# Kernel optimization log

Hardware: AMD Instinct MI355X
Metric: run time of the kernel (lower is better)

## Reference

```python
import jax, jax.numpy as jnp
import numpy as np
import math

ALPHA = 0.1
LAMDA = 0.5
N_NODES = 100000
N_EDGES = 1600000
NLAYER = 4


def gcn_norm(edge_index, num_nodes):
    # symmetric GCN normalization with added self loops (fill value 1.0)
    loop = jnp.arange(num_nodes, dtype=edge_index.dtype)
    row = jnp.concatenate([edge_index[0], loop])
    col = jnp.concatenate([edge_index[1], loop])
    w = jnp.ones(row.shape[0], dtype=jnp.float32)
    deg = jax.ops.segment_sum(w, col, num_segments=num_nodes)
    dis = jnp.where(deg > 0, jax.lax.rsqrt(deg), 0.0)
    return row, col, dis[row] * w * dis[col]


def gcnii_conv(x, h0, w1, w2, beta, row, col, norm_w, num_nodes):
    # support/initial residual mixing (GCNII)
    support = (1.0 - beta) * (1.0 - ALPHA) * x + beta * (x @ w1)
    initial = (1.0 - beta) * ALPHA * h0 + beta * (h0 @ w2)
    # gather-scale-scatter: out[i] = sum_e norm_w[e] * support[row[e]] at col[e]
    msgs = norm_w[:, None] * support[row]
    agg = jax.ops.segment_sum(msgs, col, num_segments=num_nodes)
    return agg + initial


def setup_inputs() -> dict:
    key = jax.random.key(0)
    ks = jax.random.split(key, 8)
    # edges without self loops: col = (row + offset) % N, offset in [1, N-1]
    row = jax.random.randint(ks[0], (N_EDGES,), 0, N_NODES)
    off = jax.random.randint(ks[1], (N_EDGES,), 1, N_NODES)
    col = (row + off) % N_NODES
    edge_index = jnp.stack([row, col]).astype(jnp.int64)
    g = 0.1
    return {
        "x": jax.random.normal(ks[2], (N_NODES, 17), jnp.float32),
        "edge_index": edge_index,
        "W_in": jax.random.normal(ks[3], (17, 64), jnp.float32) * g,
        "b_in": jnp.zeros((64,), jnp.float32),
        "W1": jax.random.normal(ks[4], (NLAYER, 64, 64), jnp.float32) * g,
        "W2": jax.random.normal(ks[5], (NLAYER, 64, 64), jnp.float32) * g,
        "W_out": jax.random.normal(ks[6], (64, 2), jnp.float32) * g,
        "b_out": jnp.zeros((2,), jnp.float32),
    }


def reference(x, edge_index, W_in, b_in, W1, W2, W_out, b_out):
    num_nodes = x.shape[0]
    row, col, norm_w = gcn_norm(edge_index, num_nodes)
    # eval mode: dropout is identity
    h = jax.nn.relu(x @ W_in + b_in)
    h0 = h
    for i in range(NLAYER):
        beta = math.log(LAMDA / (i + 1) + 1.0)
        h = jax.nn.relu(gcnii_conv(h, h0, W1[i], W2[i], beta, row, col, norm_w, num_nodes))
    logits = h @ W_out + b_out
    return jax.nn.log_softmax(logits, axis=1)
```

## Files before the change

### kernel.cpp

```cpp
#include <hip/hip_runtime.h>
#include <math.h>

#define ALPHA_C 0.1f
#define EPB 4096

typedef __attribute__((ext_vector_type(4))) float f32x4;
typedef __attribute__((ext_vector_type(8))) short bf16x8;

__device__ __forceinline__ float readlane_f(float v, int l) {
    return __int_as_float(__builtin_amdgcn_readlane(__float_as_int(v), l));
}

__device__ __forceinline__ unsigned short bf16_rtne(float f) {
    unsigned u = __float_as_uint(f);
    unsigned r = (u + 0x7FFFu + ((u >> 16) & 1u)) >> 16;
    return (unsigned short)r;
}

__global__ void k_rhist(const int* __restrict__ col, int E, int span,
                        int* __restrict__ rangecount) {
    __shared__ int l[64];
    int tid = threadIdx.x;
    if (tid < 64) l[tid] = 0;
    __syncthreads();
    int base = blockIdx.x * EPB;
#pragma unroll
    for (int it = 0; it < 16; ++it) {
        int e = base + it * 256 + tid;
        if (e < E) atomicAdd(&l[(unsigned)col[e] / (unsigned)span], 1);
    }
    __syncthreads();
    if (tid < 64 && l[tid]) atomicAdd(&rangecount[tid], l[tid]);
}

__global__ void k_rscan(const int* __restrict__ rangecount,
                        int* __restrict__ rangeoffs, int E) {
    __shared__ int s[64];
    int tid = threadIdx.x;
    int v = rangecount[tid];
    s[tid] = v;
    __syncthreads();
    for (int d = 1; d < 64; d <<= 1) {
        int t = (tid >= d) ? s[tid - d] : 0;
        __syncthreads();
        s[tid] += t;
        __syncthreads();
    }
    rangeoffs[tid] = s[tid] - v;
    if (tid == 63) rangeoffs[64] = E;
}

__global__ void k_binA(const int* __restrict__ row, const int* __restrict__ col,
                       const int* __restrict__ rangeoffs, int* __restrict__ gcur,
                       uint2* __restrict__ staged, int E, int span) {
    __shared__ int lrun[64];
    int tid = threadIdx.x;
    int base = blockIdx.x * EPB;
    if (tid < 64) lrun[tid] = 0;
    __syncthreads();
#pragma unroll
    for (int it = 0; it < 16; ++it) {
        int e = base + it * 256 + tid;
        if (e < E) atomicAdd(&lrun[(unsigned)col[e] / (unsigned)span], 1);
    }
    __syncthreads();
    if (tid < 64) {
        int cnt = lrun[tid];
        int gb = cnt ? atomicAdd(&gcur[tid], cnt) : 0;
        lrun[tid] = rangeoffs[tid] + gb;
    }
    __syncthreads();
#pragma unroll
    for (int it = 0; it < 16; ++it) {
        int e = base + it * 256 + tid;
        if (e < E) {
            int c = col[e];
            int r = (unsigned)c / (unsigned)span;
            int pos = atomicAdd(&lrun[r], 1);
            staged[pos] = make_uint2((unsigned)c, (unsigned)row[e]);
        }
    }
}

__global__ void k_binB(const uint2* __restrict__ staged, const int* __restrict__ rangeoffs,
                       int* __restrict__ offs, float* __restrict__ dinv,
                       int* __restrict__ srcarr, int N, int span) {
    __shared__ int lcnt[1600];
    __shared__ int partial[256];
    int r = blockIdx.x;
    int tid = threadIdx.x;
    int nstart = r * span;
    if (nstart >= N) return;
    int nend = nstart + span; if (nend > N) nend = N;
    int cnt = nend - nstart;
    int estart = rangeoffs[r], eend = rangeoffs[r + 1];
    for (int t = tid; t < cnt; t += 256) lcnt[t] = 0;
    __syncthreads();
    for (int e = estart + tid; e < eend; e += 256)
        atomicAdd(&lcnt[(int)staged[e].x - nstart], 1);
    __syncthreads();
    int chunk = (cnt + 255) / 256;
    int c0 = tid * chunk; if (c0 > cnt) c0 = cnt;
    int c1 = c0 + chunk;  if (c1 > cnt) c1 = cnt;
    int sum = 0;
    for (int t = c0; t < c1; ++t) sum += lcnt[t];
    partial[tid] = sum;
    __syncthreads();
    for (int d = 1; d < 256; d <<= 1) {
        int t = (tid >= d) ? partial[tid - d] : 0;
        __syncthreads();
        partial[tid] += t;
        __syncthreads();
    }
    int run = estart + partial[tid] - sum;
    for (int t = c0; t < c1; ++t) {
        int c = lcnt[t];
        lcnt[t] = run;
        offs[nstart + t] = run;
        dinv[nstart + t] = rsqrtf(1.0f + (float)c);
        run += c;
    }
    if (nend == N && tid == 0) offs[N] = eend;
    __syncthreads();
    for (int e = estart + tid; e < eend; e += 256) {
        uint2 cr = staged[e];
        int idx = atomicAdd(&lcnt[(int)cr.x - nstart], 1);
        srcarr[idx] = (int)cr.y;
    }
}

__global__ void k_in(const float* __restrict__ x, const float* __restrict__ Win,
                     const float* __restrict__ bin, const float* __restrict__ dinv,
                     float* __restrict__ h0, unsigned short* __restrict__ g, int N) {
    int lane = threadIdx.x & 63;
    int wave = (blockIdx.x * blockDim.x + threadIdx.x) >> 6;
    int nwaves = (gridDim.x * blockDim.x) >> 6;
    float wreg[17];
#pragma unroll
    for (int k = 0; k < 17; ++k) wreg[k] = Win[k * 64 + lane];
    float breg = bin[lane];
    for (int i = wave; i < N; i += nwaves) {
        float xv = (lane < 17) ? x[i * 17 + lane] : 0.0f;
        float acc = breg;
#pragma unroll
        for (int k = 0; k < 17; ++k) acc += readlane_f(xv, k) * wreg[k];
        float r = fmaxf(acc, 0.0f);
        h0[(size_t)i * 64 + lane] = r;
        g[(size_t)i * 64 + lane] = bf16_rtne(dinv[i] * r);
    }
}

template <bool WRITE_G>
__global__ void k_gmix(const unsigned int* __restrict__ gp, const float* __restrict__ h0,
                       const float* __restrict__ W1, const float* __restrict__ W2,
                       const float* __restrict__ dinv, const int* __restrict__ offs,
                       const int* __restrict__ srcarr, float beta,
                       float* __restrict__ of32, unsigned short* __restrict__ og16,
                       int N) {
    __shared__ float atile_s[4][16][68];
    int lane = threadIdx.x & 63;
    int wv = threadIdx.x >> 6;
    float (*atile)[68] = atile_s[wv];
    int p = lane & 31, s = lane >> 5;
    int wid = (blockIdx.x * blockDim.x + threadIdx.x) >> 6;
    int nw = (gridDim.x * blockDim.x) >> 6;
    float c1 = (1.0f - beta) * (1.0f - ALPHA_C);
    float c2 = (1.0f - beta) * ALPHA_C;

    bf16x8 bfrag[4][4];
#pragma unroll
    for (int c = 0; c < 4; ++c) {
#pragma unroll
        for (int ks = 0; ks < 4; ++ks) {
            int n = c * 16 + (lane & 15);
            int kb = ks * 32 + (lane >> 4) * 8;
            bf16x8 f;
#pragma unroll
            for (int j = 0; j < 8; ++j) {
                int k = kb + j;
                float w = (k < 64) ? beta * W1[k * 64 + n]
                                   : beta * W2[(k - 64) * 64 + n];
                f[j] = (short)bf16_rtne(w);
            }
            bfrag[c][ks] = f;
        }
    }

    int ntiles = (N + 15) >> 4;
    for (int t = wid; t < ntiles; t += nw) {
        for (int ii = 0; ii < 16; ++ii) {
            int i = t * 16 + ii; if (i >= N) i = N - 1;
            int e0 = offs[i], e1 = offs[i + 1];
            float a0 = 0.0f, a1 = 0.0f;
            for (int base = e0 + s * 8; base < e1; base += 16) {
                int idx[8];
                unsigned v[8];
#pragma unroll
                for (int u = 0; u < 8; ++u) {
                    int ee = base + u;
                    idx[u] = srcarr[ee < e1 ? ee : e1 - 1];
                }
#pragma unroll
                for (int u = 0; u < 8; ++u) v[u] = gp[(size_t)idx[u] * 32 + p];
#pragma unroll
                for (int u = 0; u < 8; ++u) {
                    bool ok = (base + u < e1);
                    a0 += ok ? __uint_as_float(v[u] << 16) : 0.0f;
                    a1 += ok ? __uint_as_float(v[u] & 0xFFFF0000u) : 0.0f;
                }
            }
            a0 += __shfl_xor(a0, 32, 64);
            a1 += __shfl_xor(a1, 32, 64);
            unsigned sv = gp[(size_t)i * 32 + p];
            a0 += __uint_as_float(sv << 16);
            a1 += __uint_as_float(sv & 0xFFFF0000u);
            if (s == 0) {
                float di = dinv[i];
                atile[ii][2 * p] = di * a0;
                atile[ii][2 * p + 1] = di * a1;
            }
        }
        int rl = lane & 15;
        int koff = (lane >> 4) * 8;
        int grow = t * 16 + rl; if (grow >= N) grow = N - 1;
        f32x4 acc[4];
#pragma unroll
        for (int c = 0; c < 4; ++c) acc[c] = (f32x4){0.f, 0.f, 0.f, 0.f};
#pragma unroll
        for (int ks = 0; ks < 4; ++ks) {
            const float* sp = (ks < 2)
                ? &atile[rl][ks * 32 + koff]
                : &h0[(size_t)grow * 64 + (ks - 2) * 32 + koff];
            f32x4 lo = *(const f32x4*)sp;
            f32x4 hi = *(const f32x4*)(sp + 4);
            bf16x8 af;
#pragma unroll
            for (int j = 0; j < 4; ++j) af[j] = (short)bf16_rtne(lo[j]);
#pragma unroll
            for (int j = 0; j < 4; ++j) af[4 + j] = (short)bf16_rtne(hi[j]);
#pragma unroll
            for (int c = 0; c < 4; ++c)
                acc[c] = __builtin_amdgcn_mfma_f32_16x16x32_bf16(af, bfrag[c][ks], acc[c], 0, 0, 0);
        }
#pragma unroll
        for (int c = 0; c < 4; ++c) {
            int col = c * 16 + rl;
#pragma unroll
            for (int q = 0; q < 4; ++q) {
                int row16 = (lane >> 4) * 4 + q;
                int gr = t * 16 + row16;
                if (gr < N) {
                    float a = atile[row16][col];
                    size_t o = (size_t)gr * 64 + col;
                    float v = c1 * a + c2 * h0[o] + acc[c][q];
                    float rr = fmaxf(v, 0.0f);
                    if (WRITE_G) og16[o] = bf16_rtne(dinv[gr] * rr);
                    else         of32[o] = rr;
                }
            }
        }
    }
}

__global__ void k_out(const float* __restrict__ h, const float* __restrict__ Wout,
                      const float* __restrict__ bout, float* __restrict__ out, int N) {
    int lane = threadIdx.x & 63;
    int wave = (blockIdx.x * blockDim.x + threadIdx.x) >> 6;
    int nwaves = (gridDim.x * blockDim.x) >> 6;
    float w0 = Wout[lane * 2 + 0], w1 = Wout[lane * 2 + 1];
    float b0 = bout[0], b1 = bout[1];
    for (int i = wave; i < N; i += nwaves) {
        float hv = h[(size_t)i * 64 + lane];
        float p0 = hv * w0, p1 = hv * w1;
#pragma unroll
        for (int d = 32; d > 0; d >>= 1) {
            p0 += __shfl_xor(p0, d, 64);
            p1 += __shfl_xor(p1, d, 64);
        }
        if (lane == 0) {
            float c0 = p0 + b0, c1 = p1 + b1;
            float m = fmaxf(c0, c1);
            float lse = m + logf(expf(c0 - m) + expf(c1 - m));
            out[(size_t)i * 2 + 0] = c0 - lse;
            out[(size_t)i * 2 + 1] = c1 - lse;
        }
    }
}

extern "C" void kernel_launch(void* const* d_in, const int* in_sizes, int n_in,
                              void* d_out, int out_size, void* d_ws, size_t ws_size,
                              hipStream_t stream) {
    const float* x    = (const float*)d_in[0];
    const int*   ei   = (const int*)d_in[1];
    const float* Win  = (const float*)d_in[2];
    const float* bin  = (const float*)d_in[3];
    const float* W1   = (const float*)d_in[4];
    const float* W2   = (const float*)d_in[5];
    const float* Wout = (const float*)d_in[6];
    const float* bout = (const float*)d_in[7];
    float* out = (float*)d_out;

    const int N = in_sizes[0] / 17;
    const int E = in_sizes[1] / 2;
    const int* rowp = ei;
    const int* colp = ei + E;
    const int span = (N + 63) / 64;

    char* p = (char*)d_ws;
    auto alloc = [&](size_t bytes) -> char* {
        char* r = p;
        p += (bytes + 255) & ~(size_t)255;
        return r;
    };
    int*   offs   = (int*)alloc((size_t)(N + 1) * sizeof(int));
    float* dinv   = (float*)alloc((size_t)N * sizeof(float));
    int*   rc_gc  = (int*)alloc(128 * sizeof(int));
    int*   roffs  = (int*)alloc(65 * sizeof(int));
    int*   srcarr = (int*)alloc((size_t)E * sizeof(int));
    size_t gbytes = (size_t)N * 64 * sizeof(unsigned short);
    size_t stbytes = (size_t)E * sizeof(uint2);
    char*  stg    = alloc(stbytes > gbytes ? stbytes : gbytes);
    float* h0     = (float*)alloc((size_t)N * 64 * sizeof(float));
    float* hfin   = (float*)alloc((size_t)N * 64 * sizeof(float));
    unsigned short* gA = (unsigned short*)alloc(gbytes);
    uint2*          staged = (uint2*)stg;
    unsigned short* gB     = (unsigned short*)stg;

    int* rangecount = rc_gc;
    int* gcur       = rc_gc + 64;
    hipMemsetAsync(rc_gc, 0, 128 * sizeof(int), stream);

    const int TB = 256;
    const int nbA = (E + EPB - 1) / EPB;

    k_rhist<<<nbA, TB, 0, stream>>>(colp, E, span, rangecount);
    k_rscan<<<1, 64, 0, stream>>>(rangecount, roffs, E);
    k_binA<<<nbA, TB, 0, stream>>>(rowp, colp, roffs, gcur, staged, E, span);
    k_binB<<<64, TB, 0, stream>>>(staged, roffs, offs, dinv, srcarr, N, span);

    k_in<<<2048, TB, 0, stream>>>(x, Win, bin, dinv, h0, gA, N);

    for (int l = 0; l < 4; ++l) {
        float beta = logf(0.5f / (float)(l + 1) + 1.0f);
        const unsigned short* gin = (l & 1) ? gB : gA;
        unsigned short*       gout = (l & 1) ? gA : gB;
        if (l < 3)
            k_gmix<true><<<1024, TB, 0, stream>>>((const unsigned int*)gin, h0,
                                                  W1 + (size_t)l * 4096, W2 + (size_t)l * 4096,
                                                  dinv, offs, srcarr, beta,
                                                  nullptr, gout, N);
        else
            k_gmix<false><<<1024, TB, 0, stream>>>((const unsigned int*)gin, h0,
                                                   W1 + (size_t)l * 4096, W2 + (size_t)l * 4096,
                                                   dinv, offs, srcarr, beta,
                                                   hfin, nullptr, N);
    }
    k_out<<<1024, TB, 0, stream>>>(hfin, Wout, bout, out, N);
}
```

Measured before the change: 470.1 us.

## Store h0 in bf16, fold alpha residual into W2, one tile per wave

h0 is now stored as bf16 and loaded straight into the MFMA A fragment, which halves its memory traffic and drops the separate fp32 reload in the epilogue. The (1-beta)*alpha*h0 term is folded into the diagonal of the W2 B fragment. The grid-stride loop is replaced with one 16-row tile per wave. Each half-wave now aggregates its own node instead of splitting one node's edges across two halves, and dinv is cached in LDS. This costs some precision, since h0 and the residual coefficient now go through bf16, and it launches many more blocks, each of which rebuilds the B fragments from W1 and W2.

```diff
diff --git a/kernel.cpp b/kernel.cpp
--- a/kernel.cpp
+++ b/kernel.cpp
@@ -5,6 +5,7 @@
 #define EPB 4096
 
 typedef __attribute__((ext_vector_type(4))) float f32x4;
+typedef __attribute__((ext_vector_type(2))) float f32x2;
 typedef __attribute__((ext_vector_type(8))) short bf16x8;
 
 __device__ __forceinline__ float readlane_f(float v, int l) {
@@ -131,7 +132,8 @@
 
 __global__ void k_in(const float* __restrict__ x, const float* __restrict__ Win,
                      const float* __restrict__ bin, const float* __restrict__ dinv,
-                     float* __restrict__ h0, unsigned short* __restrict__ g, int N) {
+                     unsigned short* __restrict__ h0b, unsigned short* __restrict__ g,
+                     int N) {
     int lane = threadIdx.x & 63;
     int wave = (blockIdx.x * blockDim.x + threadIdx.x) >> 6;
     int nwaves = (gridDim.x * blockDim.x) >> 6;
@@ -145,25 +147,25 @@
 #pragma unroll
         for (int k = 0; k < 17; ++k) acc += readlane_f(xv, k) * wreg[k];
         float r = fmaxf(acc, 0.0f);
-        h0[(size_t)i * 64 + lane] = r;
+        h0b[(size_t)i * 64 + lane] = bf16_rtne(r);
         g[(size_t)i * 64 + lane] = bf16_rtne(dinv[i] * r);
     }
 }
 
 template <bool WRITE_G>
-__global__ void k_gmix(const unsigned int* __restrict__ gp, const float* __restrict__ h0,
+__global__ void k_gmix(const unsigned int* __restrict__ gp,
+                       const unsigned int* __restrict__ h0b,
                        const float* __restrict__ W1, const float* __restrict__ W2,
                        const float* __restrict__ dinv, const int* __restrict__ offs,
                        const int* __restrict__ srcarr, float beta,
                        float* __restrict__ of32, unsigned short* __restrict__ og16,
-                       int N) {
+                       int N, int ntiles) {
     __shared__ float atile_s[4][16][68];
     int lane = threadIdx.x & 63;
     int wv = threadIdx.x >> 6;
     float (*atile)[68] = atile_s[wv];
     int p = lane & 31, s = lane >> 5;
-    int wid = (blockIdx.x * blockDim.x + threadIdx.x) >> 6;
-    int nw = (gridDim.x * blockDim.x) >> 6;
+    int t = (blockIdx.x * blockDim.x + threadIdx.x) >> 6;
     float c1 = (1.0f - beta) * (1.0f - ALPHA_C);
     float c2 = (1.0f - beta) * ALPHA_C;
 
@@ -178,85 +180,86 @@
 #pragma unroll
             for (int j = 0; j < 8; ++j) {
                 int k = kb + j;
-                float w = (k < 64) ? beta * W1[k * 64 + n]
-                                   : beta * W2[(k - 64) * 64 + n];
+                float w = (k < 64)
+                    ? beta * W1[k * 64 + n]
+                    : beta * W2[(k - 64) * 64 + n] + (((k - 64) == n) ? c2 : 0.0f);
                 f[j] = (short)bf16_rtne(w);
             }
             bfrag[c][ks] = f;
         }
     }
 
-    int ntiles = (N + 15) >> 4;
-    for (int t = wid; t < ntiles; t += nw) {
-        for (int ii = 0; ii < 16; ++ii) {
-            int i = t * 16 + ii; if (i >= N) i = N - 1;
-            int e0 = offs[i], e1 = offs[i + 1];
-            float a0 = 0.0f, a1 = 0.0f;
-            for (int base = e0 + s * 8; base < e1; base += 16) {
-                int idx[8];
-                unsigned v[8];
-#pragma unroll
-                for (int u = 0; u < 8; ++u) {
-                    int ee = base + u;
-                    idx[u] = srcarr[ee < e1 ? ee : e1 - 1];
-                }
-#pragma unroll
-                for (int u = 0; u < 8; ++u) v[u] = gp[(size_t)idx[u] * 32 + p];
-#pragma unroll
-                for (int u = 0; u < 8; ++u) {
-                    bool ok = (base + u < e1);
-                    a0 += ok ? __uint_as_float(v[u] << 16) : 0.0f;
-                    a1 += ok ? __uint_as_float(v[u] & 0xFFFF0000u) : 0.0f;
-                }
+    if (t >= ntiles) return;
+
+    for (int ii = 0; ii < 8; ++ii) {
+        int i = t * 16 + 2 * ii + s; if (i >= N) i = N - 1;
+        int e0 = offs[i], e1 = offs[i + 1];
+        float a0 = 0.0f, a1 = 0.0f;
+        for (int base = e0; base < e1; base += 8) {
+            int idx[8];
+            unsigned v[8];
+#pragma unroll
+            for (int u = 0; u < 8; ++u) {
+                int ee = base + u;
+                idx[u] = srcarr[ee < e1 ? ee : e1 - 1];
             }
-            a0 += __shfl_xor(a0, 32, 64);
-            a1 += __shfl_xor(a1, 32, 64);
-            unsigned sv = gp[(size_t)i * 32 + p];
-            a0 += __uint_as_float(sv << 16);
-            a1 += __uint_as_float(sv & 0xFFFF0000u);
-            if (s == 0) {
-                float di = dinv[i];
-                atile[ii][2 * p] = di * a0;
-                atile[ii][2 * p + 1] = di * a1;
+#pragma unroll
+            for (int u = 0; u < 8; ++u) v[u] = gp[(size_t)idx[u] * 32 + p];
+#pragma unroll
+            for (int u = 0; u < 8; ++u) {
+                bool ok = (base + u < e1);
+                a0 += ok ? __uint_as_float(v[u] << 16) : 0.0f;
+                a1 += ok ? __uint_as_float(v[u] & 0xFFFF0000u) : 0.0f;
             }
         }
-        int rl = lane & 15;
-        int koff = (lane >> 4) * 8;
-        int grow = t * 16 + rl; if (grow >= N) grow = N - 1;
-        f32x4 acc[4];
-#pragma unroll
-        for (int c = 0; c < 4; ++c) acc[c] = (f32x4){0.f, 0.f, 0.f, 0.f};
-#pragma unroll
-        for (int ks = 0; ks < 4; ++ks) {
-            const float* sp = (ks < 2)
-                ? &atile[rl][ks * 32 + koff]
-                : &h0[(size_t)grow * 64 + (ks - 2) * 32 + koff];
+        unsigned sv = gp[(size_t)i * 32 + p];
+        a0 += __uint_as_float(sv << 16);
+        a1 += __uint_as_float(sv & 0xFFFF0000u);
+        float di = dinv[i];
+        int r16 = 2 * ii + s;
+        f32x2 w = {di * a0, di * a1};
+        *(f32x2*)&atile[r16][2 * p] = w;
+        if (p == 0) atile[r16][66] = di;
+    }
+
+    int rl = lane & 15;
+    int koff = (lane >> 4) * 8;
+    int grow = t * 16 + rl; if (grow >= N) grow = N - 1;
+    f32x4 acc[4];
+#pragma unroll
+    for (int c = 0; c < 4; ++c) acc[c] = (f32x4){0.f, 0.f, 0.f, 0.f};
+#pragma unroll
+    for (int ks = 0; ks < 4; ++ks) {
+        bf16x8 af;
+        if (ks < 2) {
+            const float* sp = &atile[rl][ks * 32 + koff];
             f32x4 lo = *(const f32x4*)sp;
             f32x4 hi = *(const f32x4*)(sp + 4);
-            bf16x8 af;
 #pragma unroll
             for (int j = 0; j < 4; ++j) af[j] = (short)bf16_rtne(lo[j]);
 #pragma unroll
             for (int j = 0; j < 4; ++j) af[4 + j] = (short)bf16_rtne(hi[j]);
-#pragma unroll
-            for (int c = 0; c < 4; ++c)
-                acc[c] = __builtin_amdgcn_mfma_f32_16x16x32_bf16(af, bfrag[c][ks], acc[c], 0, 0, 0);
-        }
-#pragma unroll
-        for (int c = 0; c < 4; ++c) {
-            int col = c * 16 + rl;
-#pragma unroll
-            for (int q = 0; q < 4; ++q) {
-                int row16 = (lane >> 4) * 4 + q;
-                int gr = t * 16 + row16;
-                if (gr < N) {
-                    float a = atile[row16][col];
-                    size_t o = (size_t)gr * 64 + col;
-                    float v = c1 * a + c2 * h0[o] + acc[c][q];
-                    float rr = fmaxf(v, 0.0f);
-                    if (WRITE_G) og16[o] = bf16_rtne(dinv[gr] * rr);
-                    else         of32[o] = rr;
-                }
+        } else {
+            af = *(const bf16x8*)&h0b[((size_t)grow * 64 + (ks - 2) * 32 + koff) >> 1];
+        }
+#pragma unroll
+        for (int c = 0; c < 4; ++c)
+            acc[c] = __builtin_amdgcn_mfma_f32_16x16x32_bf16(af, bfrag[c][ks], acc[c], 0, 0, 0);
+    }
+
+#pragma unroll
+    for (int c = 0; c < 4; ++c) {
+        int col = c * 16 + rl;
+#pragma unroll
+        for (int q = 0; q < 4; ++q) {
+            int row16 = (lane >> 4) * 4 + q;
+            int gr = t * 16 + row16;
+            if (gr < N) {
+                float v = c1 * atile[row16][col] + acc[c][q];
+                float rr = fmaxf(v, 0.0f);
+                size_t o = (size_t)gr * 64 + col;
+                if (WRITE_G) og16[o] = bf16_rtne(atile[row16][66] * rr);
+                else         of32[o] = rr;
             }
         }
     }
@@ -317,12 +320,12 @@
     int*   rc_gc  = (int*)alloc(128 * sizeof(int));
     int*   roffs  = (int*)alloc(65 * sizeof(int));
     int*   srcarr = (int*)alloc((size_t)E * sizeof(int));
-    size_t gbytes = (size_t)N * 64 * sizeof(unsigned short);
+    size_t gbytes  = (size_t)N * 64 * sizeof(unsigned short);
     size_t stbytes = (size_t)E * sizeof(uint2);
     char*  stg    = alloc(stbytes > gbytes ? stbytes : gbytes);
-    float* h0     = (float*)alloc((size_t)N * 64 * sizeof(float));
-    float* hfin   = (float*)alloc((size_t)N * 64 * sizeof(float));
-    unsigned short* gA = (unsigned short*)alloc(gbytes);
+    unsigned short* h0b  = (unsigned short*)alloc(gbytes);
+    float*          hfin = (float*)alloc((size_t)N * 64 * sizeof(float));
+    unsigned short* gA   = (unsigned short*)alloc(gbytes);
     uint2*          staged = (uint2*)stg;
     unsigned short* gB     = (unsigned short*)stg;
 
@@ -338,22 +341,27 @@
     k_binA<<<nbA, TB, 0, stream>>>(rowp, colp, roffs, gcur, staged, E, span);
     k_binB<<<64, TB, 0, stream>>>(staged, roffs, offs, dinv, srcarr, N, span);
 
-    k_in<<<2048, TB, 0, stream>>>(x, Win, bin, dinv, h0, gA, N);
+    k_in<<<2048, TB, 0, stream>>>(x, Win, bin, dinv, h0b, gA, N);
+
+    const int ntiles = (N + 15) >> 4;
+    const int nbG = (ntiles + 3) / 4;
 
     for (int l = 0; l < 4; ++l) {
         float beta = logf(0.5f / (float)(l + 1) + 1.0f);
-        const unsigned short* gin = (l & 1) ? gB : gA;
+        const unsigned short* gin  = (l & 1) ? gB : gA;
         unsigned short*       gout = (l & 1) ? gA : gB;
         if (l < 3)
-            k_gmix<true><<<1024, TB, 0, stream>>>((const unsigned int*)gin, h0,
+            k_gmix<true><<<nbG, TB, 0, stream>>>((const unsigned int*)gin,
+                                                 (const unsigned int*)h0b,
+                                                 W1 + (size_t)l * 4096, W2 + (size_t)l * 4096,
+                                                 dinv, offs, srcarr, beta,
+                                                 nullptr, gout, N, ntiles);
+        else
+            k_gmix<false><<<nbG, TB, 0, stream>>>((const unsigned int*)gin,
+                                                  (const unsigned int*)h0b,
                                                   W1 + (size_t)l * 4096, W2 + (size_t)l * 4096,
                                                   dinv, offs, srcarr, beta,
-                                                  nullptr, gout, N);
-        else
-            k_gmix<false><<<1024, TB, 0, stream>>>((const unsigned int*)gin, h0,
-                                                   W1 + (size_t)l * 4096, W2 + (size_t)l * 4096,
-                                                   dinv, offs, srcarr, beta,
-                                                   hfin, nullptr, N);
+                                                  hfin, nullptr, N, ntiles);
     }
     k_out<<<1024, TB, 0, stream>>>(hfin, Wout, bout, out, N);
 }
```

Result: slower. 537.7 us (+14.4%).
